# Kernel tuning notes

Measured on AMD Instinct MI355X. Metric: run time of the kernel, lower is better.

Reference implementation:

```python
import jax, jax.numpy as jnp
import numpy as np

B, N_PER_GRAPH = 16, 512          # uniform graphs -> to_dense_batch is a reshape
N_TOKENS = B * N_PER_GRAPH
M = 32                            # neighbors per node
D_MODEL, D_EDGE, H = 256, 128, 8


def _layernorm(x, g, b, eps=1e-5):
    m = jnp.mean(x, axis=-1, keepdims=True)
    v = jnp.mean((x - m) ** 2, axis=-1, keepdims=True)
    return (x - m) * jax.lax.rsqrt(v + eps) * g + b


def _frame_ops():
    # 2^3 = 8 sign-flip operations, matches FrameAveraging.create_ops
    d = jnp.array([-1.0, 1.0], dtype=jnp.float32)
    g = jnp.meshgrid(d, d, d, indexing='ij')
    return jnp.stack(g, axis=-1).reshape(8, 3)


def _forward(token_embs, geo_feats, edge_feats, neighbor_indices, neighbor_masks,
             ln_qkv_g, ln_qkv_b, W_qkv, b_qkv, ln_e_g, ln_e_b, W_qkv_e, b_qkv_e,
             w_attn, w_edge, W_gate, b_gate, W_fc1, b_fc1, ln_h_g, ln_h_b,
             W_fc2, b_fc2, W_fa, b_fa):
    n = token_embs.shape[0]
    d_head = D_MODEL // H
    de_head = D_EDGE // H
    # qkv transformation
    qkv = _layernorm(token_embs, ln_qkv_g, ln_qkv_b) @ W_qkv + b_qkv
    q, k, v = [a.reshape(n, H, d_head) for a in jnp.split(qkv, 3, axis=-1)]
    qkve = _layernorm(edge_feats, ln_e_g, ln_e_b) @ W_qkv_e + b_qkv_e
    qe, ve = [a.reshape(n, M, H, de_head) for a in jnp.split(qkve, 2, axis=-1)]
    gate = jax.nn.sigmoid(token_embs @ W_gate + b_gate)            # [n,1]
    # GAT-style MLP attention over gathered neighbors
    message = q[:, None] + k[neighbor_indices]                     # [n,M,H,d]
    attn = jnp.einsum('nmhd,d->nmh', message, w_attn) \
         + jnp.einsum('nmhe,e->nmh', qe, w_edge)
    attn = jnp.where(neighbor_masks[..., None], attn, -1e9)
    attn = jax.nn.softmax(jnp.transpose(attn, (0, 2, 1)), axis=-1)  # [n,H,M]
    # context aggregation
    v_n = v[neighbor_indices]                                      # [n,M,H,d]
    scalar_ctx = jnp.einsum('nhm,nmhd->nhd', attn, v_n).reshape(n, -1)
    edge_ctx = jnp.einsum('nhm,nmhd->nhd', attn, ve).reshape(n, -1)
    hcat = jnp.concatenate([scalar_ctx, edge_ctx], axis=-1)
    hmid = _layernorm(jax.nn.gelu(hcat @ W_fc1 + b_fc1, approximate=False), ln_h_g, ln_h_b)
    scalar_out = hmid @ W_fc2 + b_fc2 + token_embs
    # geometric branch with frame averaging (n_heads > 1 path)
    Xb = geo_feats.reshape(B, N_PER_GRAPH, 3)                      # dense batch, full mask
    center = Xb.mean(axis=1)                                       # [B,3]
    Xc = Xb - center[:, None]
    C = jax.lax.stop_gradient(jnp.einsum('bni,bnj->bij', Xc, Xc))  # backward=False -> detach
    _, V = jnp.linalg.eigh(C)                                      # symmetric, UPLO irrelevant
    ops = _frame_ops()
    F_ops = jax.lax.stop_gradient(ops[None, :, None, :] * V[:, None])  # [B,8,3,3]
    h_fr = jnp.einsum('bpj,boji->bopi', Xc, F_ops)                 # [B,8,N,3]
    geo_f = jnp.transpose(h_fr, (1, 0, 2, 3)).reshape(8, n, 3)     # frame-major, node order b*N+p
    geo_neigh = geo_f[:, neighbor_indices]                         # [8,n,M,3]
    geo_ctx = jnp.einsum('nhm,fnmd->fnhd', attn, geo_neigh)        # [8,n,H,3]
    agg = jax.nn.silu(jnp.einsum('fnhd,h->fnd', geo_ctx, W_fa) + b_fa)  # W_frame_agg
    geo_b = jnp.transpose(agg, (1, 0, 2)).reshape(B, N_PER_GRAPH, 8, 3)
    geo_b = jnp.transpose(geo_b, (0, 2, 1, 3))                     # [B,8,N,3]
    inv = jnp.einsum('boij,bopj->bopi', F_ops, geo_b).mean(axis=1) + center[:, None]
    geo_context = inv.reshape(n, 3)
    geo_out = geo_context * gate + geo_feats * (1.0 - gate)
    return scalar_out, geo_out


def setup_inputs() -> dict:
    key = jax.random.key(0)
    ks = jax.random.split(key, 16)
    r = lambda k, shape, s=0.02: (jax.random.normal(k, shape) * s).astype(jnp.float32)
    token_embs = jax.random.normal(ks[0], (N_TOKENS, D_MODEL), dtype=jnp.float32)
    geo_feats = jax.random.normal(ks[1], (N_TOKENS, 3), dtype=jnp.float32)
    edge_feats = jax.random.normal(ks[2], (N_TOKENS, M, D_EDGE), dtype=jnp.float32)
    base = (jnp.arange(N_TOKENS) // N_PER_GRAPH) * N_PER_GRAPH
    neighbor_indices = base[:, None] + jax.random.randint(ks[3], (N_TOKENS, M), 0, N_PER_GRAPH)
    batch_idx = jnp.arange(N_TOKENS) // N_PER_GRAPH
    neighbor_masks = jax.random.uniform(ks[4], (N_TOKENS, M)) < 0.9
    d_head, de_head = D_MODEL // H, D_EDGE // H
    return dict(
        token_embs=token_embs, geo_feats=geo_feats, edge_feats=edge_feats,
        neighbor_indices=neighbor_indices, batch_idx=batch_idx, neighbor_masks=neighbor_masks,
        ln_qkv_g=jnp.ones(D_MODEL), ln_qkv_b=jnp.zeros(D_MODEL),
        W_qkv=r(ks[5], (D_MODEL, 3 * D_MODEL)), b_qkv=jnp.zeros(3 * D_MODEL),
        ln_e_g=jnp.ones(D_EDGE), ln_e_b=jnp.zeros(D_EDGE),
        W_qkv_e=r(ks[6], (D_EDGE, 2 * D_EDGE)), b_qkv_e=jnp.zeros(2 * D_EDGE),
        w_attn=r(ks[7], (d_head,), 0.1), w_edge=r(ks[8], (de_head,), 0.1),
        W_gate=jnp.zeros((D_MODEL, 1)), b_gate=jnp.ones((1,)),   # _init_params
        W_fc1=r(ks[9], (D_MODEL + D_EDGE, D_MODEL)), b_fc1=jnp.zeros(D_MODEL),
        ln_h_g=jnp.ones(D_MODEL), ln_h_b=jnp.zeros(D_MODEL),
        W_fc2=r(ks[10], (D_MODEL, D_MODEL)), b_fc2=jnp.zeros(D_MODEL),
        W_fa=r(ks[11], (H,), 0.3), b_fa=jnp.zeros((1,)),
    )


def reference(token_embs, geo_feats, edge_feats, neighbor_indices, batch_idx, neighbor_masks,
              ln_qkv_g, ln_qkv_b, W_qkv, b_qkv, ln_e_g, ln_e_b, W_qkv_e, b_qkv_e,
              w_attn, w_edge, W_gate, b_gate, W_fc1, b_fc1, ln_h_g, ln_h_b,
              W_fc2, b_fc2, W_fa, b_fa):
    # batch_idx is uniform (arange // N_PER_GRAPH); dense batching handled by reshape
    return _forward(token_embs, geo_feats, edge_feats, neighbor_indices, neighbor_masks,
                    ln_qkv_g, ln_qkv_b, W_qkv, b_qkv, ln_e_g, ln_e_b, W_qkv_e, b_qkv_e,
                    w_attn, w_edge, W_gate, b_gate, W_fc1, b_fc1, ln_h_g, ln_h_b,
                    W_fc2, b_fc2, W_fa, b_fa)
```

## Files before the change

kernel.cpp:

```cpp
#include <hip/hip_runtime.h>
#include <math.h>

#define NTOK 8192
#define NPG  512
#define MNEI 32
#define DM   256
#define DE   128
#define NH   8

#define OFF_WCAT  0u
#define OFF_BCAT  69632u
#define OFF_WEF   69904u
#define OFF_BEF   70928u
#define OFF_FLAG  70936u
#define OFF_QA    70944u
#define OFF_KA    136480u
#define OFF_GATE  202016u
#define OFF_VW    210208u
#define OFF_PROJ  2307360u
#define OFF_VMAT  2331936u
#define OFF_CEN   2332080u
#define OFF_HCAT  2332128u

#define OUT_GEO_OFF 2097152

__device__ __forceinline__ void fma4x4(const float4 a, const float4 w, float4* acc) {
    acc[0].x += a.x*w.x; acc[0].y += a.x*w.y; acc[0].z += a.x*w.z; acc[0].w += a.x*w.w;
    acc[1].x += a.y*w.x; acc[1].y += a.y*w.y; acc[1].z += a.y*w.z; acc[1].w += a.y*w.w;
    acc[2].x += a.z*w.x; acc[2].y += a.z*w.y; acc[2].z += a.z*w.z; acc[2].w += a.z*w.w;
    acc[3].x += a.w*w.x; acc[3].y += a.w*w.y; acc[3].z += a.w*w.z; acc[3].w += a.w*w.w;
}

__global__ __launch_bounds__(256) void k_fold(
    const float* __restrict__ Wqkv, const float* __restrict__ bqkv,
    const float* __restrict__ Wqkve, const float* __restrict__ bqkve,
    const float* __restrict__ w_attn, const float* __restrict__ w_edge,
    const int* __restrict__ maskp, float* __restrict__ ws)
{
    int t = threadIdx.x;
    if (blockIdx.x == 0) {
        __shared__ int sbad, sflt;
        if (t == 0) { sbad = 0; sflt = 0; }
        __syncthreads();
        int bad = 0, flt = 0;
        for (int i = 0; i < 256; i++) {
            unsigned int w = (unsigned int)maskp[i*256 + t];
            if (w > 1u) bad = 1;
            if (w == 0x3F800000u) flt = 1;
        }
        if (bad) atomicOr(&sbad, 1);
        if (flt) atomicOr(&sflt, 1);
        __syncthreads();
        if (t == 0) {
            int f = sflt ? 2 : (sbad ? 1 : 0);
            ((int*)(ws + OFF_FLAG))[0] = f;
        }
        return;
    }
    int gid = (blockIdx.x - 1) * 256 + t;
    if (gid < 69632) {
        int r = gid / 272, c = gid % 272;
        float val;
        if (c < 16) {
            int h = c & 7; int off = (c < 8) ? 0 : 256;
            float s = 0.f;
            for (int d = 0; d < 32; d++) s += Wqkv[r*768 + off + h*32 + d] * w_attn[d];
            val = s;
        } else {
            val = Wqkv[r*768 + 512 + (c - 16)];
        }
        ws[OFF_WCAT + gid] = val;
    } else if (gid < 69632 + 272) {
        int c = gid - 69632;
        float val;
        if (c < 16) {
            int h = c & 7; int off = (c < 8) ? 0 : 256;
            float s = 0.f;
            for (int d = 0; d < 32; d++) s += bqkv[off + h*32 + d] * w_attn[d];
            val = s;
        } else {
            val = bqkv[512 + (c - 16)];
        }
        ws[OFF_BCAT + c] = val;
    } else if (gid < 69904 + 1024) {
        int i = gid - 69904;
        int h = i >> 7, r = i & 127;
        float s = 0.f;
        for (int e = 0; e < 16; e++) s += Wqkve[r*256 + h*16 + e] * w_edge[e];
        ws[OFF_WEF + i] = s;
    } else if (gid < 70928 + 8) {
        int h = gid - 70928;
        float s = 0.f;
        for (int e = 0; e < 16; e++) s += bqkve[h*16 + e] * w_edge[e];
        ws[OFF_BEF + h] = s;
    }
}

__global__ __launch_bounds__(320) void k_tokprep(
    const float* __restrict__ tok, const float* __restrict__ ln_g,
    const float* __restrict__ ln_b, const float* __restrict__ Wgate,
    const float* __restrict__ bgate, float* __restrict__ ws)
{
    __shared__ __align__(16) float sln[256 * 20];
    int t = threadIdx.x;
    int tok0 = blockIdx.x * 16;

    for (int idx = t; idx < 4096; idx += 320) {
        int tt = idx >> 8, k = idx & 255;
        sln[k*20 + tt] = tok[(size_t)(tok0 + tt) * 256 + k];
    }
    __syncthreads();

    int wave = t >> 6, lane = t & 63;
    if (wave < 4) {
        for (int rr = 0; rr < 4; rr++) {
            int tt = wave * 4 + rr;
            float s = 0.f, gdot = 0.f;
            float xs[4];
            for (int q = 0; q < 4; q++) {
                int k = lane + 64*q;
                float x = sln[k*20 + tt];
                xs[q] = x; s += x; gdot += x * Wgate[k];
            }
            for (int m = 32; m >= 1; m >>= 1) { s += __shfl_xor(s,m,64); gdot += __shfl_xor(gdot,m,64); }
            float mu = s * (1.0f/256.0f);
            float vs = 0.f;
            for (int q = 0; q < 4; q++) { float d = xs[q]-mu; vs += d*d; }
            for (int m = 32; m >= 1; m >>= 1) vs += __shfl_xor(vs,m,64);
            float rinv = rsqrtf(vs*(1.0f/256.0f)+1e-5f);
            for (int q = 0; q < 4; q++) {
                int k = lane + 64*q;
                sln[k*20 + tt] = (xs[q]-mu)*rinv*ln_g[k] + ln_b[k];
            }
            if (lane == 0) ws[OFF_GATE + tok0 + tt] = 1.0f/(1.0f+expf(-(gdot + bgate[0])));
        }
    }
    __syncthreads();

    if (t < 272) {
        int i = t / 68, j = t - i*68;
        const float* Wc = ws + OFF_WCAT + 4*j;
        float4 acc[4];
        acc[0] = acc[1] = acc[2] = acc[3] = make_float4(0.f,0.f,0.f,0.f);
        #pragma unroll 4
        for (int k = 0; k < 256; k++) {
            float4 a4 = *(const float4*)&sln[k*20 + 4*i];
            float4 w4 = *(const float4*)&Wc[(size_t)k*272];
            fma4x4(a4, w4, acc);
        }
        float4 b4 = *(const float4*)&ws[OFF_BCAT + 4*j];
        for (int ti = 0; ti < 4; ti++) {
            int n = tok0 + 4*i + ti;
            float4 v = acc[ti];
            v.x += b4.x; v.y += b4.y; v.z += b4.z; v.w += b4.w;
            if (j >= 4) {
                *(float4*)&ws[OFF_VW + (size_t)n*256 + (4*j - 16)] = v;
            } else {
                float vv[4] = {v.x, v.y, v.z, v.w};
                for (int c = 0; c < 4; c++) {
                    int col = 4*j + c;
                    if (col < 8) ws[OFF_QA + n*8 + col] = vv[c];
                    else         ws[OFF_KA + n*8 + (col-8)] = vv[c];
                }
            }
        }
    }
}

__global__ __launch_bounds__(256) void k_geo(const float* __restrict__ geo, float* __restrict__ ws)
{
    __shared__ float sred[4 * 9];
    __shared__ float sres[9];
    __shared__ float sV[9];
    int t = threadIdx.x, g = blockIdx.x;
    int wave = t >> 6, lane = t & 63;
    const float* gp = geo + (size_t)g * NPG * 3;

    float x0[2], y0[2], z0[2];
    float sx = 0.f, sy = 0.f, sz = 0.f;
    for (int i = 0; i < 2; i++) {
        int p = t + 256 * i;
        x0[i] = gp[p*3 + 0]; y0[i] = gp[p*3 + 1]; z0[i] = gp[p*3 + 2];
        sx += x0[i]; sy += y0[i]; sz += z0[i];
    }
    {
        float vals[3] = {sx, sy, sz};
        for (int q = 0; q < 3; q++) {
            float v = vals[q];
            for (int m = 32; m >= 1; m >>= 1) v += __shfl_xor(v, m, 64);
            if (lane == 0) sred[wave*9 + q] = v;
        }
    }
    __syncthreads();
    if (t < 3) {
        float s = 0.f;
        for (int w = 0; w < 4; w++) s += sred[w*9 + t];
        sres[t] = s * (1.0f / 512.0f);
    }
    __syncthreads();
    float cx = sres[0], cy = sres[1], cz = sres[2];

    float c6[6] = {0.f, 0.f, 0.f, 0.f, 0.f, 0.f};
    for (int i = 0; i < 2; i++) {
        float dx = x0[i] - cx, dy = y0[i] - cy, dz = z0[i] - cz;
        c6[0] += dx*dx; c6[1] += dx*dy; c6[2] += dx*dz;
        c6[3] += dy*dy; c6[4] += dy*dz; c6[5] += dz*dz;
    }
    for (int q = 0; q < 6; q++) {
        float v = c6[q];
        for (int m = 32; m >= 1; m >>= 1) v += __shfl_xor(v, m, 64);
        if (lane == 0) sred[wave*9 + q] = v;
    }
    __syncthreads();
    if (t < 6) {
        float s = 0.f;
        for (int w = 0; w < 4; w++) s += sred[w*9 + t];
        sres[t] = s;
    }
    __syncthreads();

    if (t == 0) {
        double a[3][3];
        a[0][0] = sres[0]; a[0][1] = a[1][0] = sres[1]; a[0][2] = a[2][0] = sres[2];
        a[1][1] = sres[3]; a[1][2] = a[2][1] = sres[4]; a[2][2] = sres[5];
        double v[3][3] = {{1,0,0},{0,1,0},{0,0,1}};
        const int ps[3] = {0, 0, 1}, qs[3] = {1, 2, 2};
        for (int sweep = 0; sweep < 10; sweep++) {
            for (int pi = 0; pi < 3; pi++) {
                int p = ps[pi], q = qs[pi];
                double apq = a[p][q];
                if (fabs(apq) < 1e-300) continue;
                double theta = (a[q][q] - a[p][p]) / (2.0 * apq);
                double tt = ((theta >= 0.0) ? 1.0 : -1.0) / (fabs(theta) + sqrt(theta*theta + 1.0));
                double c = 1.0 / sqrt(tt*tt + 1.0), s = tt * c;
                int k = 3 - p - q;
                double app = a[p][p], aqq = a[q][q], akp = a[k][p], akq = a[k][q];
                a[p][p] = app - tt * apq;
                a[q][q] = aqq + tt * apq;
                a[p][q] = 0.0; a[q][p] = 0.0;
                a[k][p] = c*akp - s*akq; a[p][k] = a[k][p];
                a[k][q] = s*akp + c*akq; a[q][k] = a[k][q];
                for (int kk = 0; kk < 3; kk++) {
                    double vp = v[kk][p], vq = v[kk][q];
                    v[kk][p] = c*vp - s*vq;
                    v[kk][q] = s*vp + c*vq;
                }
            }
        }
        for (int r = 0; r < 3; r++)
            for (int c2 = 0; c2 < 3; c2++) {
                float fv = (float)v[r][c2];
                sV[r*3 + c2] = fv;
                ws[OFF_VMAT + g*9 + r*3 + c2] = fv;
            }
        ws[OFF_CEN + g*3 + 0] = cx;
        ws[OFF_CEN + g*3 + 1] = cy;
        ws[OFF_CEN + g*3 + 2] = cz;
    }
    __syncthreads();

    for (int i = 0; i < 2; i++) {
        int p = t + 256 * i;
        float dx = x0[i] - cx, dy = y0[i] - cy, dz = z0[i] - cz;
        for (int c = 0; c < 3; c++) {
            float pr = dx * sV[0*3 + c] + dy * sV[1*3 + c] + dz * sV[2*3 + c];
            ws[OFF_PROJ + (size_t)(g*NPG + p)*3 + c] = pr;
        }
    }
}

__global__ __launch_bounds__(256) void k_attn(
    const float* __restrict__ edge, const int* __restrict__ nbr,
    const void* __restrict__ maskp,
    const float* __restrict__ lneg, const float* __restrict__ lneb,
    const float* __restrict__ bqkve, const float* __restrict__ Wqkve,
    const float* __restrict__ Wfa, const float* __restrict__ bfa,
    const float* __restrict__ geo, float* __restrict__ ws, float* __restrict__ out)
{
    __shared__ __align__(16) float se[32 * 132];
    __shared__ __align__(16) float swe[8 * 132];
    __shared__ __align__(16) float sew[8 * 132];
    __shared__ __align__(16) float sattn[8 * 36];
    __shared__ __align__(16) float sq[64 * 4];
    __shared__ int   snbr[32];
    __shared__ int   smask[32];
    __shared__ float sqa[8], sbef[8];
    __shared__ float sge[128], sbe[128];
    __shared__ float sg3[4];

    int t = threadIdx.x;
    int n = blockIdx.x;
    int g = n >> 9;
    int flag = ((const int*)(ws + OFF_FLAG))[0];

    if (t < 32) {
        snbr[t] = nbr[n*32 + t];
        int mv;
        if (flag == 1)      mv = (int)((const unsigned char*)maskp)[n*32 + t];
        else if (flag == 2) mv = (((const float*)maskp)[n*32 + t] != 0.0f) ? 1 : 0;
        else                mv = ((const int*)maskp)[n*32 + t];
        smask[t] = mv;
    }
    if (t < 8) { sqa[t] = ws[OFF_QA + n*8 + t]; sbef[t] = ws[OFF_BEF + t]; }
    if (t >= 32 && t < 160) { sge[t - 32] = lneg[t - 32]; sbe[t - 32] = lneb[t - 32]; }
    {
        int idx = t * 4;
        int h = idx >> 7, r = idx & 127;
        *(float4*)&swe[h*132 + r] = *(const float4*)&ws[OFF_WEF + idx];
    }
    {
        const float4* ep = (const float4*)(edge + (size_t)n * 4096);
        for (int j = 0; j < 4; j++) {
            int l = j*1024 + t*4;
            float4 v4 = ep[l >> 2];
            int m = l >> 7, r = l & 127;
            *(float4*)&se[m*132 + r] = v4;
        }
    }
    __syncthreads();

    {
        int m = t >> 3, sub = t & 7;
        int base = m*132 + sub*16;
        float4 x0 = *(float4*)&se[base + 0];
        float4 x1 = *(float4*)&se[base + 4];
        float4 x2 = *(float4*)&se[base + 8];
        float4 x3 = *(float4*)&se[base + 12];
        float s = x0.x+x0.y+x0.z+x0.w + x1.x+x1.y+x1.z+x1.w
                + x2.x+x2.y+x2.z+x2.w + x3.x+x3.y+x3.z+x3.w;
        for (int mm = 4; mm >= 1; mm >>= 1) s += __shfl_xor(s, mm, 8);
        float mu = s * (1.0f / 128.0f);
        float vs = (x0.x-mu)*(x0.x-mu) + (x0.y-mu)*(x0.y-mu) + (x0.z-mu)*(x0.z-mu) + (x0.w-mu)*(x0.w-mu)
                 + (x1.x-mu)*(x1.x-mu) + (x1.y-mu)*(x1.y-mu) + (x1.z-mu)*(x1.z-mu) + (x1.w-mu)*(x1.w-mu)
                 + (x2.x-mu)*(x2.x-mu) + (x2.y-mu)*(x2.y-mu) + (x2.z-mu)*(x2.z-mu) + (x2.w-mu)*(x2.w-mu)
                 + (x3.x-mu)*(x3.x-mu) + (x3.y-mu)*(x3.y-mu) + (x3.z-mu)*(x3.z-mu) + (x3.w-mu)*(x3.w-mu);
        for (int mm = 4; mm >= 1; mm >>= 1) vs += __shfl_xor(vs, mm, 8);
        float rinv = rsqrtf(vs * (1.0f / 128.0f) + 1e-5f);
        int r0 = sub * 16;
        x0.x = (x0.x-mu)*rinv*sge[r0+0]  + sbe[r0+0];  x0.y = (x0.y-mu)*rinv*sge[r0+1]  + sbe[r0+1];
        x0.z = (x0.z-mu)*rinv*sge[r0+2]  + sbe[r0+2];  x0.w = (x0.w-mu)*rinv*sge[r0+3]  + sbe[r0+3];
        x1.x = (x1.x-mu)*rinv*sge[r0+4]  + sbe[r0+4];  x1.y = (x1.y-mu)*rinv*sge[r0+5]  + sbe[r0+5];
        x1.z = (x1.z-mu)*rinv*sge[r0+6]  + sbe[r0+6];  x1.w = (x1.w-mu)*rinv*sge[r0+7]  + sbe[r0+7];
        x2.x = (x2.x-mu)*rinv*sge[r0+8]  + sbe[r0+8];  x2.y = (x2.y-mu)*rinv*sge[r0+9]  + sbe[r0+9];
        x2.z = (x2.z-mu)*rinv*sge[r0+10] + sbe[r0+10]; x2.w = (x2.w-mu)*rinv*sge[r0+11] + sbe[r0+11];
        x3.x = (x3.x-mu)*rinv*sge[r0+12] + sbe[r0+12]; x3.y = (x3.y-mu)*rinv*sge[r0+13] + sbe[r0+13];
        x3.z = (x3.z-mu)*rinv*sge[r0+14] + sbe[r0+14]; x3.w = (x3.w-mu)*rinv*sge[r0+15] + sbe[r0+15];
        *(float4*)&se[base + 0]  = x0;
        *(float4*)&se[base + 4]  = x1;
        *(float4*)&se[base + 8]  = x2;
        *(float4*)&se[base + 12] = x3;
    }
    __syncthreads();

    {
        int m = t >> 3, h = t & 7;
        float acc = sbef[h];
        #pragma unroll 8
        for (int r = 0; r < 128; r += 4) {
            float4 e4 = *(float4*)&se[m*132 + r];
            float4 w4 = *(float4*)&swe[h*132 + r];
            acc += e4.x*w4.x + e4.y*w4.y + e4.z*w4.z + e4.w*w4.w;
        }
        float lg = sqa[h] + acc + ws[OFF_KA + snbr[m]*8 + h];
        if (!smask[m]) lg = -1e9f;
        sattn[h*36 + m] = lg;
    }
    __syncthreads();

    {
        int h = t >> 5, m2 = t & 31;
        float x = sattn[h*36 + m2];
        float mx = x;
        for (int mm = 16; mm >= 1; mm >>= 1) mx = fmaxf(mx, __shfl_xor(mx, mm, 32));
        float e = expf(x - mx);
        float sum = e;
        for (int mm = 16; mm >= 1; mm >>= 1) sum += __shfl_xor(sum, mm, 32);
        sattn[h*36 + m2] = e / sum;
    }
    __syncthreads();

    float4 accS = make_float4(0.f,0.f,0.f,0.f);
    if (t < 128) {
        int half = t >> 6, c4 = t & 63;
        int h = c4 >> 3;
        const float* vw = ws + OFF_VW;
        #pragma unroll 4
        for (int mi = 0; mi < 16; mi++) {
            int m = half*16 + mi;
            float a = sattn[h*36 + m];
            int row = snbr[m];
            float4 v4 = *(const float4*)&vw[(size_t)row*256 + 4*c4];
            accS.x += a*v4.x; accS.y += a*v4.y; accS.z += a*v4.z; accS.w += a*v4.w;
        }
        if (half) *(float4*)&sq[c4*4] = accS;
        if (t < 32) {
            float wmv = 0.f;
            #pragma unroll
            for (int h2 = 0; h2 < 8; h2++) wmv += Wfa[h2] * sattn[h2*36 + t];
            int row = snbr[t];
            const float* pp = ws + OFF_PROJ + (size_t)row*3;
            float q0 = wmv * pp[0], q1 = wmv * pp[1], q2 = wmv * pp[2];
            for (int st = 16; st >= 1; st >>= 1) {
                q0 += __shfl_xor(q0, st, 32);
                q1 += __shfl_xor(q1, st, 32);
                q2 += __shfl_xor(q2, st, 32);
            }
            if (t < 3) {
                float sd = (t == 0) ? q0 : (t == 1) ? q1 : q2;
                float bb = bfa[0];
                float p1 = sd + bb, p2 = -sd + bb;
                float s1v = p1 / (1.0f + expf(-p1));
                float s2v = p2 / (1.0f + expf(-p2));
                sg3[t] = 0.5f * (s1v - s2v);
            }
        }
    } else {
        int rq = t & 31, hb = (t >> 5) - 4;
        float4 e1 = make_float4(0.f,0.f,0.f,0.f);
        float4 e2 = make_float4(0.f,0.f,0.f,0.f);
        #pragma unroll
        for (int mq = 0; mq < 8; mq++) {
            float4 a4a = *(const float4*)&sattn[hb*36 + 4*mq];
            float4 a4b = *(const float4*)&sattn[(hb+4)*36 + 4*mq];
            float aa[4] = {a4a.x, a4a.y, a4a.z, a4a.w};
            float ab[4] = {a4b.x, a4b.y, a4b.z, a4b.w};
            #pragma unroll
            for (int c = 0; c < 4; c++) {
                int m = 4*mq + c;
                float4 e4 = *(const float4*)&se[m*132 + rq*4];
                e1.x += aa[c]*e4.x; e1.y += aa[c]*e4.y; e1.z += aa[c]*e4.z; e1.w += aa[c]*e4.w;
                e2.x += ab[c]*e4.x; e2.y += ab[c]*e4.y; e2.z += ab[c]*e4.z; e2.w += ab[c]*e4.w;
            }
        }
        *(float4*)&sew[hb*132 + rq*4]     = e1;
        *(float4*)&sew[(hb+4)*132 + rq*4] = e2;
    }
    __syncthreads();

    float* sec = se;
    float4 accE = make_float4(0.f,0.f,0.f,0.f);
    {
        int col4 = t & 31, rgrp = t >> 5;
        int h2 = col4 >> 2;
        const float* wqb = Wqkve + 128 + 4*col4;
        #pragma unroll 4
        for (int ri = 0; ri < 16; ri++) {
            int r = rgrp*16 + ri;
            float sv = sew[h2*132 + r];
            float4 w4 = *(const float4*)&wqb[(size_t)r*256];
            accE.x += sv*w4.x; accE.y += sv*w4.y; accE.z += sv*w4.z; accE.w += sv*w4.w;
        }
        if (t < 64) {
            float4 p = *(const float4*)&sq[t*4];
            float4 tot;
            tot.x = accS.x + p.x; tot.y = accS.y + p.y;
            tot.z = accS.z + p.z; tot.w = accS.w + p.w;
            *(float4*)&ws[OFF_HCAT + (size_t)n*384 + 4*t] = tot;
        }
        *(float4*)&sec[rgrp*128 + col4*4] = accE;
    }
    __syncthreads();

    if (t < 128) {
        float ec = bqkve[128 + t];
        #pragma unroll
        for (int g2 = 0; g2 < 8; g2++) ec += sec[g2*128 + t];
        ws[OFF_HCAT + (size_t)n*384 + 256 + t] = ec;
    }
    if (t < 3) {
        const float* Vm = ws + OFF_VMAT + g*9;
        float gc = Vm[t*3+0]*sg3[0] + Vm[t*3+1]*sg3[1] + Vm[t*3+2]*sg3[2] + ws[OFF_CEN + g*3 + t];
        float gt = ws[OFF_GATE + n];
        out[OUT_GEO_OFF + (size_t)n*3 + t] = gc * gt + geo[(size_t)n*3 + t] * (1.0f - gt);
    }
}

__global__ __launch_bounds__(256) void k_mlp(
    const float* __restrict__ tok, const float* __restrict__ Wfc1,
    const float* __restrict__ bfc1, const float* __restrict__ lnhg,
    const float* __restrict__ lnhb, const float* __restrict__ Wfc2,
    const float* __restrict__ bfc2, const float* __restrict__ ws,
    float* __restrict__ out)
{
    __shared__ __align__(16) float A[384 * 20];
    int t = threadIdx.x;
    int tok0 = blockIdx.x * 16;
    int i = t >> 6, j = t & 63;
    const float* hc = ws + OFF_HCAT;

    for (int it = 0; it < 24; it++) {
        int idx = it*256 + t;
        int tt = idx / 384;
        int k  = idx - tt*384;
        A[k*20 + tt] = hc[(size_t)tok0*384 + idx];
    }
    __syncthreads();

    float4 acc1[4];
    acc1[0] = acc1[1] = acc1[2] = acc1[3] = make_float4(0.f,0.f,0.f,0.f);
    {
        const float* wp = Wfc1 + 4*j;
        #pragma unroll 4
        for (int k = 0; k < 384; k++) {
            float4 a4 = *(const float4*)&A[k*20 + 4*i];
            float4 w4 = *(const float4*)&wp[(size_t)k*256];
            fma4x4(a4, w4, acc1);
        }
    }
    float h[4][4];
    {
        float4 b4 = *(const float4*)&bfc1[4*j];
        for (int ti = 0; ti < 4; ti++) {
            float xv[4] = {acc1[ti].x + b4.x, acc1[ti].y + b4.y, acc1[ti].z + b4.z, acc1[ti].w + b4.w};
            for (int c = 0; c < 4; c++) {
                float x = xv[c];
                h[ti][c] = 0.5f * x * (1.0f + erff(x * 0.70710678118654752f));
            }
        }
    }
    __syncthreads();

    {
        float s[4], q[4];
        for (int ti = 0; ti < 4; ti++) {
            s[ti] = h[ti][0] + h[ti][1] + h[ti][2] + h[ti][3];
            q[ti] = h[ti][0]*h[ti][0] + h[ti][1]*h[ti][1] + h[ti][2]*h[ti][2] + h[ti][3]*h[ti][3];
        }
        for (int m = 32; m >= 1; m >>= 1)
            for (int ti = 0; ti < 4; ti++) {
                s[ti] += __shfl_xor(s[ti], m, 64);
                q[ti] += __shfl_xor(q[ti], m, 64);
            }
        float4 g4 = *(const float4*)&lnhg[4*j];
        float4 b4 = *(const float4*)&lnhb[4*j];
        float gg[4] = {g4.x, g4.y, g4.z, g4.w};
        float bb[4] = {b4.x, b4.y, b4.z, b4.w};
        for (int ti = 0; ti < 4; ti++) {
            float mu = s[ti] * (1.0f/256.0f);
            float var = q[ti] * (1.0f/256.0f) - mu*mu;
            float rinv = rsqrtf(var + 1e-5f);
            for (int c = 0; c < 4; c++) {
                float hn = (h[ti][c] - mu) * rinv * gg[c] + bb[c];
                A[(4*j + c)*20 + 4*i + ti] = hn;
            }
        }
    }
    __syncthreads();

    float4 acc2[4];
    acc2[0] = acc2[1] = acc2[2] = acc2[3] = make_float4(0.f,0.f,0.f,0.f);
    {
        const float* wp = Wfc2 + 4*j;
        #pragma unroll 4
        for (int k = 0; k < 256; k++) {
            float4 a4 = *(const float4*)&A[k*20 + 4*i];
            float4 w4 = *(const float4*)&wp[(size_t)k*256];
            fma4x4(a4, w4, acc2);
        }
    }
    {
        float4 b4 = *(const float4*)&bfc2[4*j];
        for (int ti = 0; ti < 4; ti++) {
            size_t o = (size_t)(tok0 + 4*i + ti) * 256 + 4*j;
            float4 r4 = *(const float4*)&tok[o];
            float4 v;
            v.x = acc2[ti].x + b4.x + r4.x;
            v.y = acc2[ti].y + b4.y + r4.y;
            v.z = acc2[ti].z + b4.z + r4.z;
            v.w = acc2[ti].w + b4.w + r4.w;
            *(float4*)&out[o] = v;
        }
    }
}

extern "C" void kernel_launch(void* const* d_in, const int* in_sizes, int n_in,
                              void* d_out, int out_size, void* d_ws, size_t ws_size,
                              hipStream_t stream) {
    (void)in_sizes; (void)n_in; (void)out_size; (void)ws_size;
    const float* tok   = (const float*)d_in[0];
    const float* geo   = (const float*)d_in[1];
    const float* edge  = (const float*)d_in[2];
    const int*   nbr   = (const int*)d_in[3];
    const void*  maskp = d_in[5];
    const float* ln_qkv_g = (const float*)d_in[6];
    const float* ln_qkv_b = (const float*)d_in[7];
    const float* Wqkv  = (const float*)d_in[8];
    const float* bqkv  = (const float*)d_in[9];
    const float* ln_e_g = (const float*)d_in[10];
    const float* ln_e_b = (const float*)d_in[11];
    const float* Wqkve = (const float*)d_in[12];
    const float* bqkve = (const float*)d_in[13];
    const float* w_attn = (const float*)d_in[14];
    const float* w_edge = (const float*)d_in[15];
    const float* Wgate = (const float*)d_in[16];
    const float* bgate = (const float*)d_in[17];
    const float* Wfc1  = (const float*)d_in[18];
    const float* bfc1  = (const float*)d_in[19];
    const float* lnhg  = (const float*)d_in[20];
    const float* lnhb  = (const float*)d_in[21];
    const float* Wfc2  = (const float*)d_in[22];
    const float* bfc2  = (const float*)d_in[23];
    const float* Wfa   = (const float*)d_in[24];
    const float* bfa   = (const float*)d_in[25];
    float* ws  = (float*)d_ws;
    float* out = (float*)d_out;

    k_fold<<<dim3(279), dim3(256), 0, stream>>>(Wqkv, bqkv, Wqkve, bqkve, w_attn, w_edge,
                                                (const int*)maskp, ws);
    k_tokprep<<<dim3(512), dim3(320), 0, stream>>>(tok, ln_qkv_g, ln_qkv_b, Wgate, bgate, ws);
    k_geo<<<dim3(16), dim3(256), 0, stream>>>(geo, ws);
    k_attn<<<dim3(8192), dim3(256), 0, stream>>>(edge, nbr, maskp, ln_e_g, ln_e_b, bqkve,
                                                 Wqkve, Wfa, bfa, geo, ws, out);
    k_mlp<<<dim3(512), dim3(256), 0, stream>>>(tok, Wfc1, bfc1, lnhg, lnhb, Wfc2, bfc2, ws, out);
}
```

Measured before the change: 437.7 us.

## Halve token tiles, split-K the MLP GEMMs, fuse edge LN with logit dot

k_tokprep and k_mlp now process 8 tokens per block instead of 16, doubling the grid to use more CUs. The folded weight is split into a plain V matrix and a transposed q/k-attention block computed by separate waves. k_mlp splits the K dimension across two thread halves and reduces partial sums through shared memory. In k_attn, the edge layernorm now feeds the per-head edge logit dot directly from registers, with a shuffle reduction, which removes one barrier and some shared arrays. The cost is extra reduction steps and more total weight reads because of the smaller token tiles.

```diff
diff --git a/kernel.cpp b/kernel.cpp
--- a/kernel.cpp
+++ b/kernel.cpp
@@ -8,7 +8,8 @@
 #define DE   128
 #define NH   8
 
-#define OFF_WCAT  0u
+#define OFF_WV    0u
+#define OFF_WQAK  65536u
 #define OFF_BCAT  69632u
 #define OFF_WEF   69904u
 #define OFF_BEF   70928u
@@ -29,6 +30,10 @@
     acc[1].x += a.y*w.x; acc[1].y += a.y*w.y; acc[1].z += a.y*w.z; acc[1].w += a.y*w.w;
     acc[2].x += a.z*w.x; acc[2].y += a.z*w.y; acc[2].z += a.z*w.z; acc[2].w += a.z*w.w;
     acc[3].x += a.w*w.x; acc[3].y += a.w*w.y; acc[3].z += a.w*w.z; acc[3].w += a.w*w.w;
+}
+
+__device__ __forceinline__ float dot4(const float4 a, const float4 b) {
+    return a.x*b.x + a.y*b.y + a.z*b.z + a.w*b.w;
 }
 
 __global__ __launch_bounds__(256) void k_fold(
@@ -58,18 +63,16 @@
         return;
     }
     int gid = (blockIdx.x - 1) * 256 + t;
-    if (gid < 69632) {
-        int r = gid / 272, c = gid % 272;
-        float val;
-        if (c < 16) {
-            int h = c & 7; int off = (c < 8) ? 0 : 256;
-            float s = 0.f;
-            for (int d = 0; d < 32; d++) s += Wqkv[r*768 + off + h*32 + d] * w_attn[d];
-            val = s;
-        } else {
-            val = Wqkv[r*768 + 512 + (c - 16)];
-        }
-        ws[OFF_WCAT + gid] = val;
+    if (gid < 65536) {
+        int k = gid >> 8, c = gid & 255;
+        ws[OFF_WV + gid] = Wqkv[k*768 + 512 + c];
+    } else if (gid < 69632) {
+        int idx = gid - 65536;
+        int c = idx >> 8, k = idx & 255;
+        int h = c & 7; int off = (c < 8) ? 0 : 256;
+        float s = 0.f;
+        for (int d = 0; d < 32; d++) s += Wqkv[k*768 + off + h*32 + d] * w_attn[d];
+        ws[OFF_WQAK + idx] = s;
     } else if (gid < 69632 + 272) {
         int c = gid - 69632;
         float val;
@@ -96,74 +99,84 @@
     }
 }
 
-__global__ __launch_bounds__(320) void k_tokprep(
+__global__ __launch_bounds__(256) void k_tokprep(
     const float* __restrict__ tok, const float* __restrict__ ln_g,
     const float* __restrict__ ln_b, const float* __restrict__ Wgate,
     const float* __restrict__ bgate, float* __restrict__ ws)
 {
-    __shared__ __align__(16) float sln[256 * 20];
+    __shared__ __align__(16) float sln[256 * 12];
     int t = threadIdx.x;
-    int tok0 = blockIdx.x * 16;
-
-    for (int idx = t; idx < 4096; idx += 320) {
-        int tt = idx >> 8, k = idx & 255;
-        sln[k*20 + tt] = tok[(size_t)(tok0 + tt) * 256 + k];
-    }
+    int tok0 = blockIdx.x * 8;
+
+    #pragma unroll
+    for (int q = 0; q < 8; q++)
+        sln[t*12 + q] = tok[(size_t)(tok0 + q) * 256 + t];
     __syncthreads();
 
     int wave = t >> 6, lane = t & 63;
-    if (wave < 4) {
-        for (int rr = 0; rr < 4; rr++) {
-            int tt = wave * 4 + rr;
-            float s = 0.f, gdot = 0.f;
-            float xs[4];
-            for (int q = 0; q < 4; q++) {
-                int k = lane + 64*q;
-                float x = sln[k*20 + tt];
-                xs[q] = x; s += x; gdot += x * Wgate[k];
-            }
-            for (int m = 32; m >= 1; m >>= 1) { s += __shfl_xor(s,m,64); gdot += __shfl_xor(gdot,m,64); }
-            float mu = s * (1.0f/256.0f);
-            float vs = 0.f;
-            for (int q = 0; q < 4; q++) { float d = xs[q]-mu; vs += d*d; }
-            for (int m = 32; m >= 1; m >>= 1) vs += __shfl_xor(vs,m,64);
-            float rinv = rsqrtf(vs*(1.0f/256.0f)+1e-5f);
-            for (int q = 0; q < 4; q++) {
-                int k = lane + 64*q;
-                sln[k*20 + tt] = (xs[q]-mu)*rinv*ln_g[k] + ln_b[k];
-            }
-            if (lane == 0) ws[OFF_GATE + tok0 + tt] = 1.0f/(1.0f+expf(-(gdot + bgate[0])));
-        }
-    }
-    __syncthreads();
-
-    if (t < 272) {
-        int i = t / 68, j = t - i*68;
-        const float* Wc = ws + OFF_WCAT + 4*j;
+    for (int rr = 0; rr < 2; rr++) {
+        int tt = wave * 2 + rr;
+        float s = 0.f, gdot = 0.f;
+        float xs[4];
+        #pragma unroll
+        for (int q = 0; q < 4; q++) {
+            int k = lane + 64*q;
+            float x = sln[k*12 + tt];
+            xs[q] = x; s += x; gdot += x * Wgate[k];
+        }
+        for (int m = 32; m >= 1; m >>= 1) { s += __shfl_xor(s,m,64); gdot += __shfl_xor(gdot,m,64); }
+        float mu = s * (1.0f/256.0f);
+        float vs = 0.f;
+        #pragma unroll
+        for (int q = 0; q < 4; q++) { float d = xs[q]-mu; vs += d*d; }
+        for (int m = 32; m >= 1; m >>= 1) vs += __shfl_xor(vs,m,64);
+        float rinv = rsqrtf(vs*(1.0f/256.0f)+1e-5f);
+        #pragma unroll
+        for (int q = 0; q < 4; q++) {
+            int k = lane + 64*q;
+            sln[k*12 + tt] = (xs[q]-mu)*rinv*ln_g[k] + ln_b[k];
+        }
+        if (lane == 0) ws[OFF_GATE + tok0 + tt] = 1.0f/(1.0f+expf(-(gdot + bgate[0])));
+    }
+    __syncthreads();
+
+    if (t < 128) {
+        int i = t >> 6, j = t & 63;
+        const float* Wc = ws + OFF_WV + 4*j;
         float4 acc[4];
         acc[0] = acc[1] = acc[2] = acc[3] = make_float4(0.f,0.f,0.f,0.f);
-        #pragma unroll 4
+        #pragma unroll 8
         for (int k = 0; k < 256; k++) {
-            float4 a4 = *(const float4*)&sln[k*20 + 4*i];
-            float4 w4 = *(const float4*)&Wc[(size_t)k*272];
+            float4 a4 = *(const float4*)&sln[k*12 + 4*i];
+            float4 w4 = *(const float4*)&Wc[(size_t)k*256];
             fma4x4(a4, w4, acc);
         }
-        float4 b4 = *(const float4*)&ws[OFF_BCAT + 4*j];
+        float4 b4 = *(const float4*)&ws[OFF_BCAT + 16 + 4*j];
+        #pragma unroll
         for (int ti = 0; ti < 4; ti++) {
             int n = tok0 + 4*i + ti;
             float4 v = acc[ti];
             v.x += b4.x; v.y += b4.y; v.z += b4.z; v.w += b4.w;
-            if (j >= 4) {
-                *(float4*)&ws[OFF_VW + (size_t)n*256 + (4*j - 16)] = v;
-            } else {
-                float vv[4] = {v.x, v.y, v.z, v.w};
-                for (int c = 0; c < 4; c++) {
-                    int col = 4*j + c;
-                    if (col < 8) ws[OFF_QA + n*8 + col] = vv[c];
-                    else         ws[OFF_KA + n*8 + (col-8)] = vv[c];
-                }
-            }
-        }
+            *(float4*)&ws[OFF_VW + (size_t)n*256 + 4*j] = v;
+        }
+    } else {
+        int wave3 = (t >> 6) - 2;
+        int col = t & 15, tp = (t & 63) >> 4;
+        int tokn = wave3*4 + tp;
+        const float* wq = ws + OFF_WQAK + col*256;
+        float acc = 0.f;
+        #pragma unroll 8
+        for (int k4 = 0; k4 < 64; k4++) {
+            float4 w4 = *(const float4*)&wq[4*k4];
+            acc += w4.x * sln[(4*k4+0)*12 + tokn]
+                 + w4.y * sln[(4*k4+1)*12 + tokn]
+                 + w4.z * sln[(4*k4+2)*12 + tokn]
+                 + w4.w * sln[(4*k4+3)*12 + tokn];
+        }
+        acc += ws[OFF_BCAT + col];
+        int n = tok0 + tokn;
+        if (col < 8) ws[OFF_QA + n*8 + col] = acc;
+        else         ws[OFF_KA + n*8 + (col - 8)] = acc;
     }
 }
 
@@ -278,14 +291,12 @@
     const float* __restrict__ geo, float* __restrict__ ws, float* __restrict__ out)
 {
     __shared__ __align__(16) float se[32 * 132];
-    __shared__ __align__(16) float swe[8 * 132];
+    __shared__ __align__(16) float uSWE[8 * 132];
     __shared__ __align__(16) float sew[8 * 132];
     __shared__ __align__(16) float sattn[8 * 36];
-    __shared__ __align__(16) float sq[64 * 4];
     __shared__ int   snbr[32];
     __shared__ int   smask[32];
     __shared__ float sqa[8], sbef[8];
-    __shared__ float sge[128], sbe[128];
     __shared__ float sg3[4];
 
     int t = threadIdx.x;
@@ -302,14 +313,15 @@
         smask[t] = mv;
     }
     if (t < 8) { sqa[t] = ws[OFF_QA + n*8 + t]; sbef[t] = ws[OFF_BEF + t]; }
-    if (t >= 32 && t < 160) { sge[t - 32] = lneg[t - 32]; sbe[t - 32] = lneb[t - 32]; }
     {
         int idx = t * 4;
         int h = idx >> 7, r = idx & 127;
-        *(float4*)&swe[h*132 + r] = *(const float4*)&ws[OFF_WEF + idx];
+        int sub = r >> 4, c = r & 15;
+        *(float4*)&uSWE[sub*132 + h*16 + c] = *(const float4*)&ws[OFF_WEF + idx];
     }
     {
         const float4* ep = (const float4*)(edge + (size_t)n * 4096);
+        #pragma unroll
         for (int j = 0; j < 4; j++) {
             int l = j*1024 + t*4;
             float4 v4 = ep[l >> 2];
@@ -319,8 +331,8 @@
     }
     __syncthreads();
 
-    {
-        int m = t >> 3, sub = t & 7;
+    int m = t >> 3, sub = t & 7;
+    {
         int base = m*132 + sub*16;
         float4 x0 = *(float4*)&se[base + 0];
         float4 x1 = *(float4*)&se[base + 4];
@@ -336,34 +348,41 @@
                  + (x3.x-mu)*(x3.x-mu) + (x3.y-mu)*(x3.y-mu) + (x3.z-mu)*(x3.z-mu) + (x3.w-mu)*(x3.w-mu);
         for (int mm = 4; mm >= 1; mm >>= 1) vs += __shfl_xor(vs, mm, 8);
         float rinv = rsqrtf(vs * (1.0f / 128.0f) + 1e-5f);
-        int r0 = sub * 16;
-        x0.x = (x0.x-mu)*rinv*sge[r0+0]  + sbe[r0+0];  x0.y = (x0.y-mu)*rinv*sge[r0+1]  + sbe[r0+1];
-        x0.z = (x0.z-mu)*rinv*sge[r0+2]  + sbe[r0+2];  x0.w = (x0.w-mu)*rinv*sge[r0+3]  + sbe[r0+3];
-        x1.x = (x1.x-mu)*rinv*sge[r0+4]  + sbe[r0+4];  x1.y = (x1.y-mu)*rinv*sge[r0+5]  + sbe[r0+5];
-        x1.z = (x1.z-mu)*rinv*sge[r0+6]  + sbe[r0+6];  x1.w = (x1.w-mu)*rinv*sge[r0+7]  + sbe[r0+7];
-        x2.x = (x2.x-mu)*rinv*sge[r0+8]  + sbe[r0+8];  x2.y = (x2.y-mu)*rinv*sge[r0+9]  + sbe[r0+9];
-        x2.z = (x2.z-mu)*rinv*sge[r0+10] + sbe[r0+10]; x2.w = (x2.w-mu)*rinv*sge[r0+11] + sbe[r0+11];
-        x3.x = (x3.x-mu)*rinv*sge[r0+12] + sbe[r0+12]; x3.y = (x3.y-mu)*rinv*sge[r0+13] + sbe[r0+13];
-        x3.z = (x3.z-mu)*rinv*sge[r0+14] + sbe[r0+14]; x3.w = (x3.w-mu)*rinv*sge[r0+15] + sbe[r0+15];
+        const float4* gp4 = (const float4*)(lneg + sub*16);
+        const float4* bp4 = (const float4*)(lneb + sub*16);
+        float4 g0 = gp4[0], g1 = gp4[1], g2 = gp4[2], g3 = gp4[3];
+        float4 b0 = bp4[0], b1 = bp4[1], b2 = bp4[2], b3 = bp4[3];
+        x0.x=(x0.x-mu)*rinv*g0.x+b0.x; x0.y=(x0.y-mu)*rinv*g0.y+b0.y;
+        x0.z=(x0.z-mu)*rinv*g0.z+b0.z; x0.w=(x0.w-mu)*rinv*g0.w+b0.w;
+        x1.x=(x1.x-mu)*rinv*g1.x+b1.x; x1.y=(x1.y-mu)*rinv*g1.y+b1.y;
+        x1.z=(x1.z-mu)*rinv*g1.z+b1.z; x1.w=(x1.w-mu)*rinv*g1.w+b1.w;
+        x2.x=(x2.x-mu)*rinv*g2.x+b2.x; x2.y=(x2.y-mu)*rinv*g2.y+b2.y;
+        x2.z=(x2.z-mu)*rinv*g2.z+b2.z; x2.w=(x2.w-mu)*rinv*g2.w+b2.w;
+        x3.x=(x3.x-mu)*rinv*g3.x+b3.x; x3.y=(x3.y-mu)*rinv*g3.y+b3.y;
+        x3.z=(x3.z-mu)*rinv*g3.z+b3.z; x3.w=(x3.w-mu)*rinv*g3.w+b3.w;
         *(float4*)&se[base + 0]  = x0;
         *(float4*)&se[base + 4]  = x1;
         *(float4*)&se[base + 8]  = x2;
         *(float4*)&se[base + 12] = x3;
-    }
-    __syncthreads();
-
-    {
-        int m = t >> 3, h = t & 7;
-        float acc = sbef[h];
-        #pragma unroll 8
-        for (int r = 0; r < 128; r += 4) {
-            float4 e4 = *(float4*)&se[m*132 + r];
-            float4 w4 = *(float4*)&swe[h*132 + r];
-            acc += e4.x*w4.x + e4.y*w4.y + e4.z*w4.z + e4.w*w4.w;
-        }
-        float lg = sqa[h] + acc + ws[OFF_KA + snbr[m]*8 + h];
+
+        float accl[8];
+        const float* wb = &uSWE[sub*132];
+        #pragma unroll
+        for (int h = 0; h < 8; h++) {
+            const float4* wp = (const float4*)(wb + h*16);
+            accl[h] = dot4(x0,wp[0]) + dot4(x1,wp[1]) + dot4(x2,wp[2]) + dot4(x3,wp[3]);
+        }
+        #pragma unroll
+        for (int st = 1; st < 8; st <<= 1) {
+            #pragma unroll
+            for (int h = 0; h < 8; h++) accl[h] += __shfl_xor(accl[h], st, 8);
+        }
+        float myacc = accl[0];
+        #pragma unroll
+        for (int h = 1; h < 8; h++) myacc = (sub == h) ? accl[h] : myacc;
+        float lg = sqa[sub] + sbef[sub] + myacc + ws[OFF_KA + snbr[m]*8 + sub];
         if (!smask[m]) lg = -1e9f;
-        sattn[h*36 + m] = lg;
+        sattn[sub*36 + m] = lg;
     }
     __syncthreads();
 
@@ -379,6 +398,8 @@
     }
     __syncthreads();
 
+    float* sq = uSWE;
+
     float4 accS = make_float4(0.f,0.f,0.f,0.f);
     if (t < 128) {
         int half = t >> 6, c4 = t & 63;
@@ -386,9 +407,9 @@
         const float* vw = ws + OFF_VW;
         #pragma unroll 4
         for (int mi = 0; mi < 16; mi++) {
-            int m = half*16 + mi;
-            float a = sattn[h*36 + m];
-            int row = snbr[m];
+            int mm2 = half*16 + mi;
+            float a = sattn[h*36 + mm2];
+            int row = snbr[mm2];
             float4 v4 = *(const float4*)&vw[(size_t)row*256 + 4*c4];
             accS.x += a*v4.x; accS.y += a*v4.y; accS.z += a*v4.z; accS.w += a*v4.w;
         }
@@ -426,8 +447,8 @@
             float ab[4] = {a4b.x, a4b.y, a4b.z, a4b.w};
             #pragma unroll
             for (int c = 0; c < 4; c++) {
-                int m = 4*mq + c;
-                float4 e4 = *(const float4*)&se[m*132 + rq*4];
+                int mm2 = 4*mq + c;
+                float4 e4 = *(const float4*)&se[mm2*132 + rq*4];
                 e1.x += aa[c]*e4.x; e1.y += aa[c]*e4.y; e1.z += aa[c]*e4.z; e1.w += aa[c]*e4.w;
                 e2.x += ab[c]*e4.x; e2.y += ab[c]*e4.y; e2.z += ab[c]*e4.z; e2.w += ab[c]*e4.w;
             }
@@ -482,17 +503,19 @@
     const float* __restrict__ bfc2, const float* __restrict__ ws,
     float* __restrict__ out)
 {
-    __shared__ __align__(16) float A[384 * 20];
+    __shared__ __align__(16) float A[384 * 12];
+    __shared__ __align__(16) float R[128 * 16];
     int t = threadIdx.x;
-    int tok0 = blockIdx.x * 16;
-    int i = t >> 6, j = t & 63;
+    int tok0 = blockIdx.x * 8;
+    int i2 = (t >> 6) & 1, kh = t >> 7, j = t & 63;
     const float* hc = ws + OFF_HCAT;
 
-    for (int it = 0; it < 24; it++) {
-        int idx = it*256 + t;
+    #pragma unroll
+    for (int q = 0; q < 12; q++) {
+        int idx = q*256 + t;
         int tt = idx / 384;
         int k  = idx - tt*384;
-        A[k*20 + tt] = hc[(size_t)tok0*384 + idx];
+        A[k*12 + tt] = hc[(size_t)tok0*384 + idx];
     }
     __syncthreads();
 
@@ -500,48 +523,61 @@
     acc1[0] = acc1[1] = acc1[2] = acc1[3] = make_float4(0.f,0.f,0.f,0.f);
     {
         const float* wp = Wfc1 + 4*j;
-        #pragma unroll 4
-        for (int k = 0; k < 384; k++) {
-            float4 a4 = *(const float4*)&A[k*20 + 4*i];
+        int kbase = kh * 192;
+        #pragma unroll 8
+        for (int kk = 0; kk < 192; kk++) {
+            int k = kbase + kk;
+            float4 a4 = *(const float4*)&A[k*12 + 4*i2];
             float4 w4 = *(const float4*)&wp[(size_t)k*256];
             fma4x4(a4, w4, acc1);
         }
     }
+    if (kh == 1) {
+        int rowid = t - 128;
+        #pragma unroll
+        for (int ti = 0; ti < 4; ti++) *(float4*)&R[rowid*16 + ti*4] = acc1[ti];
+    }
+    __syncthreads();
+
     float h[4][4];
-    {
+    if (kh == 0) {
         float4 b4 = *(const float4*)&bfc1[4*j];
+        #pragma unroll
         for (int ti = 0; ti < 4; ti++) {
-            float xv[4] = {acc1[ti].x + b4.x, acc1[ti].y + b4.y, acc1[ti].z + b4.z, acc1[ti].w + b4.w};
+            float4 p = *(const float4*)&R[t*16 + ti*4];
+            float xv[4] = {acc1[ti].x + p.x + b4.x, acc1[ti].y + p.y + b4.y,
+                           acc1[ti].z + p.z + b4.z, acc1[ti].w + p.w + b4.w};
+            #pragma unroll
             for (int c = 0; c < 4; c++) {
                 float x = xv[c];
                 h[ti][c] = 0.5f * x * (1.0f + erff(x * 0.70710678118654752f));
             }
         }
-    }
-    __syncthreads();
-
-    {
-        float s[4], q[4];
+        float s[4], qv[4];
+        #pragma unroll
         for (int ti = 0; ti < 4; ti++) {
-            s[ti] = h[ti][0] + h[ti][1] + h[ti][2] + h[ti][3];
-            q[ti] = h[ti][0]*h[ti][0] + h[ti][1]*h[ti][1] + h[ti][2]*h[ti][2] + h[ti][3]*h[ti][3];
+            s[ti]  = h[ti][0] + h[ti][1] + h[ti][2] + h[ti][3];
+            qv[ti] = h[ti][0]*h[ti][0] + h[ti][1]*h[ti][1] + h[ti][2]*h[ti][2] + h[ti][3]*h[ti][3];
         }
         for (int m = 32; m >= 1; m >>= 1)
+            #pragma unroll
             for (int ti = 0; ti < 4; ti++) {
-                s[ti] += __shfl_xor(s[ti], m, 64);
-                q[ti] += __shfl_xor(q[ti], m, 64);
+                s[ti]  += __shfl_xor(s[ti], m, 64);
+                qv[ti] += __shfl_xor(qv[ti], m, 64);
             }
         float4 g4 = *(const float4*)&lnhg[4*j];
-        float4 b4 = *(const float4*)&lnhb[4*j];
+        float4 b42 = *(const float4*)&lnhb[4*j];
         float gg[4] = {g4.x, g4.y, g4.z, g4.w};
-        float bb[4] = {b4.x, b4.y, b4.z, b4.w};
+        float bb[4] = {b42.x, b42.y, b42.z, b42.w};
+        #pragma unroll
         for (int ti = 0; ti < 4; ti++) {
             float mu = s[ti] * (1.0f/256.0f);
-            float var = q[ti] * (1.0f/256.0f) - mu*mu;
+            float var = qv[ti] * (1.0f/256.0f) - mu*mu;
             float rinv = rsqrtf(var + 1e-5f);
+            #pragma unroll
             for (int c = 0; c < 4; c++) {
                 float hn = (h[ti][c] - mu) * rinv * gg[c] + bb[c];
-                A[(4*j + c)*20 + 4*i + ti] = hn;
+                A[(4*j + c)*12 + 4*i2 + ti] = hn;
             }
         }
     }
@@ -551,23 +587,34 @@
     acc2[0] = acc2[1] = acc2[2] = acc2[3] = make_float4(0.f,0.f,0.f,0.f);
     {
         const float* wp = Wfc2 + 4*j;
-        #pragma unroll 4
-        for (int k = 0; k < 256; k++) {
-            float4 a4 = *(const float4*)&A[k*20 + 4*i];
+        int kbase = kh * 128;
+        #pragma unroll 8
+        for (int kk = 0; kk < 128; kk++) {
+            int k = kbase + kk;
+            float4 a4 = *(const float4*)&A[k*12 + 4*i2];
             float4 w4 = *(const float4*)&wp[(size_t)k*256];
             fma4x4(a4, w4, acc2);
         }
     }
-    {
+    if (kh == 1) {
+        int rowid = t - 128;
+        #pragma unroll
+        for (int ti = 0; ti < 4; ti++) *(float4*)&R[rowid*16 + ti*4] = acc2[ti];
+    }
+    __syncthreads();
+
+    if (kh == 0) {
         float4 b4 = *(const float4*)&bfc2[4*j];
+        #pragma unroll
         for (int ti = 0; ti < 4; ti++) {
-            size_t o = (size_t)(tok0 + 4*i + ti) * 256 + 4*j;
+            float4 p = *(const float4*)&R[t*16 + ti*4];
+            size_t o = (size_t)(tok0 + 4*i2 + ti) * 256 + 4*j;
             float4 r4 = *(const float4*)&tok[o];
             float4 v;
-            v.x = acc2[ti].x + b4.x + r4.x;
-            v.y = acc2[ti].y + b4.y + r4.y;
-            v.z = acc2[ti].z + b4.z + r4.z;
-            v.w = acc2[ti].w + b4.w + r4.w;
+            v.x = acc2[ti].x + p.x + b4.x + r4.x;
+            v.y = acc2[ti].y + p.y + b4.y + r4.y;
+            v.z = acc2[ti].z + p.z + b4.z + r4.z;
+            v.w = acc2[ti].w + p.w + b4.w + r4.w;
             *(float4*)&out[o] = v;
         }
     }
@@ -607,9 +654,9 @@
 
     k_fold<<<dim3(279), dim3(256), 0, stream>>>(Wqkv, bqkv, Wqkve, bqkve, w_attn, w_edge,
                                                 (const int*)maskp, ws);
-    k_tokprep<<<dim3(512), dim3(320), 0, stream>>>(tok, ln_qkv_g, ln_qkv_b, Wgate, bgate, ws);
+    k_tokprep<<<dim3(1024), dim3(256), 0, stream>>>(tok, ln_qkv_g, ln_qkv_b, Wgate, bgate, ws);
     k_geo<<<dim3(16), dim3(256), 0, stream>>>(geo, ws);
     k_attn<<<dim3(8192), dim3(256), 0, stream>>>(edge, nbr, maskp, ln_e_g, ln_e_b, bqkve,
                                                  Wqkve, Wfa, bfa, geo, ws, out);
-    k_mlp<<<dim3(512), dim3(256), 0, stream>>>(tok, Wfc1, bfc1, lnhg, lnhb, Wfc2, bfc2, ws, out);
-}
+    k_mlp<<<dim3(1024), dim3(256), 0, stream>>>(tok, Wfc1, bfc1, lnhg, lnhb, Wfc2, bfc2, ws, out);
+}
```

After: 398.6 us. -8.9%, faster.
